# Performance work log

Measured on AMD Instinct MI355X. Metric: run time of the kernel, lower is better.

Reference implementation:

```python
import jax, jax.numpy as jnp
import numpy as np

N_NODES = 100000
N_FEAT = 256
HIDDEN = 16
N_CLASSES = 16
N_EDGES = 3200000


def setup_inputs() -> dict:
    key = jax.random.key(0)
    k = jax.random.split(key, 7)
    x = jax.random.normal(k[0], (N_NODES, N_FEAT), dtype=jnp.float32)
    edge_index = jax.random.randint(k[1], (2, N_EDGES), 0, N_NODES, dtype=jnp.int32)
    # GCNConv: linear (no bias) + bias added after aggregation
    s1 = 1.0 / np.sqrt(N_FEAT)
    W1 = jax.random.uniform(k[2], (N_FEAT, HIDDEN), jnp.float32, -s1, s1)
    b1 = jnp.zeros((HIDDEN,), jnp.float32)
    # SAGEConv: lin_l (on aggregated neighbors, with bias) + lin_r (root)
    s2 = 1.0 / np.sqrt(HIDDEN)
    Wl = jax.random.uniform(k[3], (HIDDEN, N_CLASSES), jnp.float32, -s2, s2)
    Wr = jax.random.uniform(k[4], (HIDDEN, N_CLASSES), jnp.float32, -s2, s2)
    b2 = jax.random.uniform(k[5], (N_CLASSES,), jnp.float32, -s2, s2)
    return {"x": x, "edge_index": edge_index, "W1": W1, "b1": b1,
            "Wl": Wl, "Wr": Wr, "b2": b2}


def reference(x, edge_index, W1, b1, Wl, Wr, b2):
    N = x.shape[0]
    src, dst = edge_index[0], edge_index[1]

    # ---- GCNConv(num_features -> hidden): transform, add self-loops,
    # symmetric normalization, sum-aggregate, add bias ----
    h = x @ W1  # [N, H]
    loop = jnp.arange(N, dtype=src.dtype)
    src2 = jnp.concatenate([src, loop])
    dst2 = jnp.concatenate([dst, loop])
    ones = jnp.ones(src2.shape[0], dtype=h.dtype)
    deg = jax.ops.segment_sum(ones, dst2, num_segments=N)  # in-degree incl. self-loop
    dinv = jnp.where(deg > 0, jax.lax.rsqrt(deg), 0.0)
    norm = dinv[src2] * dinv[dst2]  # [E+N]
    msgs = h[src2] * norm[:, None]
    h1 = jax.ops.segment_sum(msgs, dst2, num_segments=N) + b1  # [N, H]

    # ---- SAGEConv(hidden -> num_classes, aggr='mean') ----
    cnt = jax.ops.segment_sum(jnp.ones(src.shape[0], dtype=h1.dtype), dst, num_segments=N)
    agg = jax.ops.segment_sum(h1[src], dst, num_segments=N)
    agg = agg / jnp.maximum(cnt, 1.0)[:, None]  # mean over neighbors
    out = agg @ Wl + h1 @ Wr + b2  # [N, C]

    return jax.nn.log_softmax(out, axis=1)
```

## Files before the change

kernel.cpp:

```cpp
#include <hip/hip_runtime.h>
#include <cstddef>

#define NF 256
#define NH 16
#define NC 16

#define BN    128
#define BSH   7
#define BMSK  127
#define CAP   4608
#define AVLEN 32
#define ACH   (256*AVLEN)
#define NBMAX 800

typedef __attribute__((ext_vector_type(8))) short bf16x8;
typedef __attribute__((ext_vector_type(4))) float f32x4;

__device__ inline short f2bf(float f) {
    union { float f; unsigned int u; } v; v.f = f;
    const unsigned int r = v.u + 0x7FFFu + ((v.u >> 16) & 1u);
    return (short)(r >> 16);
}
__device__ inline float bf2f(unsigned short u) {
    union { unsigned int i; float f; } v; v.i = ((unsigned int)u) << 16;
    return v.f;
}

__global__ __launch_bounds__(256) void bucketA_kernel(
    const int* __restrict__ src, const int* __restrict__ dst,
    unsigned int* __restrict__ bfill, unsigned int* __restrict__ bpairs,
    int E, int NBK)
{
    __shared__ unsigned int hist[NBMAX];
    __shared__ unsigned int sbase[NBMAX];
    __shared__ unsigned int gpos[NBMAX];
    __shared__ unsigned int tmp[1024];
    __shared__ unsigned int reorder[ACH];
    __shared__ unsigned short wbid[ACH];

    const int tid = threadIdx.x;
    for (int i = tid; i < NBMAX; i += 256) hist[i] = 0u;
    __syncthreads();

    const int base = blockIdx.x * ACH;
    unsigned int pv[AVLEN];
    unsigned int ps[AVLEN];
    #pragma unroll
    for (int l = 0; l < AVLEN; ++l) {
        const int e = base + l * 256 + tid;
        if (e < E) {
            const unsigned int s = (unsigned int)src[e];
            const unsigned int d = (unsigned int)dst[e];
            const unsigned int b = d >> BSH;
            pv[l] = (s << BSH) | (d & BMSK);
            const unsigned int slot = atomicAdd(&hist[b], 1u);
            ps[l] = (slot << 10) | b;
        } else {
            ps[l] = 0xFFFFFFFFu;
        }
    }
    __syncthreads();

    for (int i = tid; i < 1024; i += 256) tmp[i] = (i < NBK) ? hist[i] : 0u;
    __syncthreads();
    for (int off = 1; off < 1024; off <<= 1) {
        unsigned int v0 = 0, v1 = 0, v2 = 0, v3 = 0;
        const int i0 = tid, i1 = tid + 256, i2 = tid + 512, i3 = tid + 768;
        if (i0 >= off) v0 = tmp[i0 - off];
        if (i1 >= off) v1 = tmp[i1 - off];
        if (i2 >= off) v2 = tmp[i2 - off];
        if (i3 >= off) v3 = tmp[i3 - off];
        __syncthreads();
        tmp[i0] += v0; tmp[i1] += v1; tmp[i2] += v2; tmp[i3] += v3;
        __syncthreads();
    }
    for (int i = tid; i < NBK; i += 256) {
        const unsigned int h = hist[i];
        sbase[i] = tmp[i] - h;
        if (h) gpos[i] = atomicAdd(&bfill[i], h);
    }
    const int cc = (base + ACH <= E) ? ACH : (E - base);
    __syncthreads();

    #pragma unroll
    for (int l = 0; l < AVLEN; ++l) {
        if (ps[l] != 0xFFFFFFFFu) {
            const unsigned int b = ps[l] & 1023u;
            const unsigned int i = sbase[b] + (ps[l] >> 10);
            reorder[i] = pv[l];
            wbid[i] = (unsigned short)b;
        }
    }
    __syncthreads();

    for (int i = tid; i < cc; i += 256) {
        const unsigned int b = wbid[i];
        const unsigned int g = gpos[b] + ((unsigned int)i - sbase[b]);
        if (g < CAP) bpairs[(size_t)b * CAP + g] = reorder[i];
    }
}

__global__ __launch_bounds__(256) void bucketB_kernel(
    const unsigned int* __restrict__ bfill, unsigned int* __restrict__ bpairs,
    int* __restrict__ rowptr, int* __restrict__ cnt, float* __restrict__ dinv,
    int N)
{
    __shared__ unsigned int pairs[CAP];
    __shared__ unsigned int ssorted[CAP];
    __shared__ unsigned int hist[BN];
    __shared__ unsigned int scan[BN];
    __shared__ unsigned int cursor[BN];

    const int tid = threadIdx.x;
    const int b = blockIdx.x;
    const size_t bbase = (size_t)b * CAP;
    unsigned int m = bfill[b]; if (m > CAP) m = CAP;

    if (tid < BN) hist[tid] = 0u;
    __syncthreads();

    for (unsigned int i = tid; i < m; i += 256) {
        const unsigned int p = bpairs[bbase + i];
        pairs[i] = p;
        atomicAdd(&hist[p & BMSK], 1u);
    }
    __syncthreads();

    if (tid < BN) scan[tid] = hist[tid];
    __syncthreads();
    for (int off = 1; off < BN; off <<= 1) {
        unsigned int v = 0;
        if (tid < BN && tid >= off) v = scan[tid - off];
        __syncthreads();
        if (tid < BN) scan[tid] += v;
        __syncthreads();
    }
    if (tid < BN) cursor[tid] = scan[tid] - hist[tid];
    __syncthreads();

    for (unsigned int i = tid; i < m; i += 256) {
        const unsigned int p = pairs[i];
        const unsigned int pos = atomicAdd(&cursor[p & BMSK], 1u);
        ssorted[pos] = p >> BSH;
    }
    __syncthreads();

    for (unsigned int i = tid; i < m; i += 256)
        bpairs[bbase + i] = ssorted[i];

    if (tid < BN) {
        const int n = b * BN + tid;
        if (n < N) {
            const unsigned int h = hist[tid];
            cnt[n] = (int)h;
            dinv[n] = rsqrtf((float)h + 1.0f);
            rowptr[n] = (int)(b * CAP + (scan[tid] - h));
        }
    }
}

__global__ __launch_bounds__(256) void gemm1_mfma_kernel(
    const float* __restrict__ x, const float* __restrict__ W1,
    const float* __restrict__ dinv, unsigned short* __restrict__ hs_bf, int N)
{
    const int lane = threadIdx.x & 63;
    const int wave = threadIdx.x >> 6;
    const int quad = lane >> 4;
    const int mn   = lane & 15;

    bf16x8 bfrag[8];
    #pragma unroll
    for (int kc = 0; kc < 8; ++kc) {
        #pragma unroll
        for (int j = 0; j < 8; ++j) {
            const int k = kc * 32 + quad * 8 + j;
            bfrag[kc][j] = f2bf(W1[k * NH + mn]);
        }
    }

    const int tile = blockIdx.x * 4 + wave;
    if (tile * 16 >= N) return;
    const int n0 = tile * 16;

    f32x4 acc = {0.f, 0.f, 0.f, 0.f};
    const float* xrow = x + (size_t)(n0 + mn) * NF + quad * 8;
    #pragma unroll
    for (int kc = 0; kc < 8; ++kc) {
        const float4 lo = *(const float4*)(xrow + kc * 32);
        const float4 hi = *(const float4*)(xrow + kc * 32 + 4);
        bf16x8 af;
        af[0] = f2bf(lo.x); af[1] = f2bf(lo.y); af[2] = f2bf(lo.z); af[3] = f2bf(lo.w);
        af[4] = f2bf(hi.x); af[5] = f2bf(hi.y); af[6] = f2bf(hi.z); af[7] = f2bf(hi.w);
        acc = __builtin_amdgcn_mfma_f32_16x16x32_bf16(af, bfrag[kc], acc, 0, 0, 0);
    }

    const float4 dv = *(const float4*)(dinv + n0 + quad * 4);
    const float d[4] = {dv.x, dv.y, dv.z, dv.w};
    #pragma unroll
    for (int r = 0; r < 4; ++r) {
        const int row = quad * 4 + r;
        hs_bf[(size_t)(n0 + row) * NH + mn] = (unsigned short)f2bf(acc[r] * d[r]);
    }
}

__global__ __launch_bounds__(256) void gcn_gather_kernel(
    const unsigned short* __restrict__ hs_bf, const unsigned int* __restrict__ csrc,
    const int* __restrict__ rowptr, const int* __restrict__ cnt,
    const float* __restrict__ dinv, const float* __restrict__ b1,
    unsigned short* __restrict__ h1_bf, int N)
{
    const int tid = threadIdx.x;
    const int n = blockIdx.x * 16 + (tid >> 4);
    if (n >= N) return;
    const int j = tid & 15;
    const int start = rowptr[n];
    const int end = start + cnt[n];

    float acc = bf2f(hs_bf[(size_t)n * NH + j]);
    int k = start;
    for (; k + 16 <= end; k += 16) {
        const int myi = (int)csrc[k + j];
        float s = 0.f;
        #pragma unroll
        for (int u = 0; u < 16; ++u) {
            const int sidx = __shfl(myi, u, 16);
            s += bf2f(hs_bf[(size_t)sidx * NH + j]);
        }
        acc += s;
    }
    for (; k < end; ++k)
        acc += bf2f(hs_bf[(size_t)csrc[k] * NH + j]);

    h1_bf[(size_t)n * NH + j] = (unsigned short)f2bf(b1[j] + dinv[n] * acc);
}

__global__ __launch_bounds__(256) void sage_out_kernel(
    const unsigned short* __restrict__ h1_bf, const unsigned int* __restrict__ csrc,
    const int* __restrict__ rowptr, const int* __restrict__ cnt,
    const float* __restrict__ Wl, const float* __restrict__ Wr,
    const float* __restrict__ b2, float* __restrict__ out, int N)
{
    __shared__ float wls[NH * NC];
    __shared__ float wrs[NH * NC];
    __shared__ float b2s[NC];
    const int tid = threadIdx.x;
    if (tid < NH * NC) { wls[tid] = Wl[tid]; wrs[tid] = Wr[tid]; }
    if (tid < NC) b2s[tid] = b2[tid];
    __syncthreads();

    const int n = blockIdx.x * 16 + (tid >> 4);
    if (n >= N) return;
    const int j = tid & 15;
    const int start = rowptr[n];
    const int deg = cnt[n];
    const int end = start + deg;

    float acc = 0.f;
    int k = start;
    for (; k + 16 <= end; k += 16) {
        const int myi = (int)csrc[k + j];
        float s = 0.f;
        #pragma unroll
        for (int u = 0; u < 16; ++u) {
            const int sidx = __shfl(myi, u, 16);
            s += bf2f(h1_bf[(size_t)sidx * NH + j]);
        }
        acc += s;
    }
    for (; k < end; ++k)
        acc += bf2f(h1_bf[(size_t)csrc[k] * NH + j]);

    const float aggj = acc / fmaxf((float)deg, 1.0f);
    const float h1j  = bf2f(h1_bf[(size_t)n * NH + j]);

    float o = b2s[j];
    #pragma unroll
    for (int kk = 0; kk < NH; ++kk) {
        const float a  = __shfl(aggj, kk, 16);
        const float hh = __shfl(h1j,  kk, 16);
        o += a * wls[kk * NC + j] + hh * wrs[kk * NC + j];
    }

    float m = o;
    #pragma unroll
    for (int off = 1; off < 16; off <<= 1) m = fmaxf(m, __shfl_xor(m, off, 16));
    const float ex = expf(o - m);
    float ssum = ex;
    #pragma unroll
    for (int off = 1; off < 16; off <<= 1) ssum += __shfl_xor(ssum, off, 16);

    out[(size_t)n * NC + j] = (o - m) - logf(ssum);
}

extern "C" void kernel_launch(void* const* d_in, const int* in_sizes, int n_in,
                              void* d_out, int out_size, void* d_ws, size_t ws_size,
                              hipStream_t stream)
{
    const float* x  = (const float*)d_in[0];
    const int*   ei = (const int*)d_in[1];
    const float* W1 = (const float*)d_in[2];
    const float* b1 = (const float*)d_in[3];
    const float* Wl = (const float*)d_in[4];
    const float* Wr = (const float*)d_in[5];
    const float* b2 = (const float*)d_in[6];
    float* out = (float*)d_out;

    const int N = in_sizes[0] / NF;
    const int E = in_sizes[1] / 2;
    const int* src = ei;
    const int* dst = ei + E;

    const int NBK = (N + BN - 1) / BN;

    unsigned short* hs_bf = (unsigned short*)d_ws;
    unsigned short* h1_bf = hs_bf + (size_t)N * NH;
    float* dinv   = (float*)(h1_bf + (size_t)N * NH);
    int*   cnt    = (int*)(dinv + N);
    int*   rowptr = cnt + N;
    unsigned int* bfill  = (unsigned int*)(rowptr + N);
    unsigned int* bpairs = bfill + 1024;

    hipMemsetAsync(bfill, 0, (size_t)NBK * sizeof(unsigned int), stream);

    bucketA_kernel<<<(E + ACH - 1) / ACH, 256, 0, stream>>>(src, dst, bfill, bpairs, E, NBK);
    bucketB_kernel<<<NBK, 256, 0, stream>>>(bfill, bpairs, rowptr, cnt, dinv, N);

    const int tiles = (N + 15) / 16;
    gemm1_mfma_kernel<<<(tiles + 3) / 4, 256, 0, stream>>>(x, W1, dinv, hs_bf, N);

    const int nodeBlk = (N + 15) / 16;
    gcn_gather_kernel<<<nodeBlk, 256, 0, stream>>>(hs_bf, bpairs, rowptr, cnt, dinv, b1, h1_bf, N);
    sage_out_kernel<<<nodeBlk, 256, 0, stream>>>(h1_bf, bpairs, rowptr, cnt, Wl, Wr, b2, out, N);
}
```

Measured before the change: 314.4 us.

## Replace per-node CSR sort with bucket-level LDS atomic aggregation

Drops the within-bucket counting sort and rowptr construction, keeping only a degree histogram pass. The two aggregation kernels now process one 128-node bucket per 512-thread block, scattering neighbor features into a shared-memory accumulator with LDS float atomics. This removes the sort's LDS work and global rewrite of bpairs, but adds LDS atomic contention and lowers the grid to about 800 blocks. It also makes float summation order nondeterministic.

```diff
diff --git a/kernel.cpp b/kernel.cpp
--- a/kernel.cpp
+++ b/kernel.cpp
@@ -100,53 +100,21 @@
     }
 }
 
-__global__ __launch_bounds__(256) void bucketB_kernel(
-    const unsigned int* __restrict__ bfill, unsigned int* __restrict__ bpairs,
-    int* __restrict__ rowptr, int* __restrict__ cnt, float* __restrict__ dinv,
-    int N)
-{
-    __shared__ unsigned int pairs[CAP];
-    __shared__ unsigned int ssorted[CAP];
+__global__ __launch_bounds__(256) void degree_kernel(
+    const unsigned int* __restrict__ bfill, const unsigned int* __restrict__ bpairs,
+    int* __restrict__ cnt, float* __restrict__ dinv, int N)
+{
     __shared__ unsigned int hist[BN];
-    __shared__ unsigned int scan[BN];
-    __shared__ unsigned int cursor[BN];
-
     const int tid = threadIdx.x;
     const int b = blockIdx.x;
+    if (tid < BN) hist[tid] = 0u;
+    __syncthreads();
+
+    unsigned int m = bfill[b]; if (m > CAP) m = CAP;
     const size_t bbase = (size_t)b * CAP;
-    unsigned int m = bfill[b]; if (m > CAP) m = CAP;
-
-    if (tid < BN) hist[tid] = 0u;
-    __syncthreads();
-
-    for (unsigned int i = tid; i < m; i += 256) {
-        const unsigned int p = bpairs[bbase + i];
-        pairs[i] = p;
-        atomicAdd(&hist[p & BMSK], 1u);
-    }
-    __syncthreads();
-
-    if (tid < BN) scan[tid] = hist[tid];
-    __syncthreads();
-    for (int off = 1; off < BN; off <<= 1) {
-        unsigned int v = 0;
-        if (tid < BN && tid >= off) v = scan[tid - off];
-        __syncthreads();
-        if (tid < BN) scan[tid] += v;
-        __syncthreads();
-    }
-    if (tid < BN) cursor[tid] = scan[tid] - hist[tid];
-    __syncthreads();
-
-    for (unsigned int i = tid; i < m; i += 256) {
-        const unsigned int p = pairs[i];
-        const unsigned int pos = atomicAdd(&cursor[p & BMSK], 1u);
-        ssorted[pos] = p >> BSH;
-    }
-    __syncthreads();
-
     for (unsigned int i = tid; i < m; i += 256)
-        bpairs[bbase + i] = ssorted[i];
+        atomicAdd(&hist[bpairs[bbase + i] & BMSK], 1u);
+    __syncthreads();
 
     if (tid < BN) {
         const int n = b * BN + tid;
@@ -154,7 +122,6 @@
             const unsigned int h = hist[tid];
             cnt[n] = (int)h;
             dinv[n] = rsqrtf((float)h + 1.0f);
-            rowptr[n] = (int)(b * CAP + (scan[tid] - h));
         }
     }
 }
@@ -203,93 +170,130 @@
     }
 }
 
-__global__ __launch_bounds__(256) void gcn_gather_kernel(
-    const unsigned short* __restrict__ hs_bf, const unsigned int* __restrict__ csrc,
-    const int* __restrict__ rowptr, const int* __restrict__ cnt,
+__global__ __launch_bounds__(512) void gcn_agg_kernel(
+    const unsigned short* __restrict__ hs_bf,
+    const unsigned int* __restrict__ bfill, const unsigned int* __restrict__ bpairs,
     const float* __restrict__ dinv, const float* __restrict__ b1,
     unsigned short* __restrict__ h1_bf, int N)
 {
+    __shared__ float acc[BN * NH];
     const int tid = threadIdx.x;
-    const int n = blockIdx.x * 16 + (tid >> 4);
-    if (n >= N) return;
+    const int b = blockIdx.x;
+    const size_t bbase = (size_t)b * CAP;
+    const int nodeBase = b * BN;
+
+    for (int t = tid; t < BN * NH; t += 512) {
+        const int n = nodeBase + (t >> 4);
+        acc[t] = (n < N) ? bf2f(hs_bf[(size_t)n * NH + (t & 15)]) : 0.f;
+    }
+    unsigned int m = bfill[b]; if (m > CAP) m = CAP;
+    __syncthreads();
+
+    const int g = tid >> 4;
     const int j = tid & 15;
-    const int start = rowptr[n];
-    const int end = start + cnt[n];
-
-    float acc = bf2f(hs_bf[(size_t)n * NH + j]);
-    int k = start;
-    for (; k + 16 <= end; k += 16) {
-        const int myi = (int)csrc[k + j];
-        float s = 0.f;
-        #pragma unroll
-        for (int u = 0; u < 16; ++u) {
-            const int sidx = __shfl(myi, u, 16);
-            s += bf2f(hs_bf[(size_t)sidx * NH + j]);
-        }
-        acc += s;
-    }
-    for (; k < end; ++k)
-        acc += bf2f(hs_bf[(size_t)csrc[k] * NH + j]);
-
-    h1_bf[(size_t)n * NH + j] = (unsigned short)f2bf(b1[j] + dinv[n] * acc);
-}
-
-__global__ __launch_bounds__(256) void sage_out_kernel(
-    const unsigned short* __restrict__ h1_bf, const unsigned int* __restrict__ csrc,
-    const int* __restrict__ rowptr, const int* __restrict__ cnt,
+    unsigned int i = g;
+    for (; i + 96 < m; i += 128) {
+        const unsigned int p0 = bpairs[bbase + i];
+        const unsigned int p1 = bpairs[bbase + i + 32];
+        const unsigned int p2 = bpairs[bbase + i + 64];
+        const unsigned int p3 = bpairs[bbase + i + 96];
+        const float v0 = bf2f(hs_bf[(size_t)(p0 >> BSH) * NH + j]);
+        const float v1 = bf2f(hs_bf[(size_t)(p1 >> BSH) * NH + j]);
+        const float v2 = bf2f(hs_bf[(size_t)(p2 >> BSH) * NH + j]);
+        const float v3 = bf2f(hs_bf[(size_t)(p3 >> BSH) * NH + j]);
+        atomicAdd(&acc[((p0 & BMSK) << 4) + j], v0);
+        atomicAdd(&acc[((p1 & BMSK) << 4) + j], v1);
+        atomicAdd(&acc[((p2 & BMSK) << 4) + j], v2);
+        atomicAdd(&acc[((p3 & BMSK) << 4) + j], v3);
+    }
+    for (; i < m; i += 32) {
+        const unsigned int p0 = bpairs[bbase + i];
+        const float v0 = bf2f(hs_bf[(size_t)(p0 >> BSH) * NH + j]);
+        atomicAdd(&acc[((p0 & BMSK) << 4) + j], v0);
+    }
+    __syncthreads();
+
+    for (int t = tid; t < BN * NH; t += 512) {
+        const int n = nodeBase + (t >> 4);
+        if (n < N)
+            h1_bf[(size_t)n * NH + (t & 15)] =
+                (unsigned short)f2bf(b1[t & 15] + dinv[n] * acc[t]);
+    }
+}
+
+__global__ __launch_bounds__(512) void sage_out_kernel(
+    const unsigned short* __restrict__ h1_bf,
+    const unsigned int* __restrict__ bfill, const unsigned int* __restrict__ bpairs,
+    const int* __restrict__ cnt,
     const float* __restrict__ Wl, const float* __restrict__ Wr,
     const float* __restrict__ b2, float* __restrict__ out, int N)
 {
+    __shared__ float acc[BN * NH];
+    __shared__ unsigned short hroot[BN * NH];
     __shared__ float wls[NH * NC];
     __shared__ float wrs[NH * NC];
     __shared__ float b2s[NC];
+
     const int tid = threadIdx.x;
+    const int b = blockIdx.x;
+    const size_t bbase = (size_t)b * CAP;
+    const int nodeBase = b * BN;
+
     if (tid < NH * NC) { wls[tid] = Wl[tid]; wrs[tid] = Wr[tid]; }
     if (tid < NC) b2s[tid] = b2[tid];
-    __syncthreads();
-
-    const int n = blockIdx.x * 16 + (tid >> 4);
-    if (n >= N) return;
+    for (int t = tid; t < BN * NH; t += 512) {
+        acc[t] = 0.f;
+        const int n = nodeBase + (t >> 4);
+        hroot[t] = (n < N) ? h1_bf[(size_t)n * NH + (t & 15)] : (unsigned short)0;
+    }
+    unsigned int m = bfill[b]; if (m > CAP) m = CAP;
+    __syncthreads();
+
+    const int g = tid >> 4;
     const int j = tid & 15;
-    const int start = rowptr[n];
-    const int deg = cnt[n];
-    const int end = start + deg;
-
-    float acc = 0.f;
-    int k = start;
-    for (; k + 16 <= end; k += 16) {
-        const int myi = (int)csrc[k + j];
-        float s = 0.f;
+    unsigned int i = g;
+    for (; i + 96 < m; i += 128) {
+        const unsigned int p0 = bpairs[bbase + i];
+        const unsigned int p1 = bpairs[bbase + i + 32];
+        const unsigned int p2 = bpairs[bbase + i + 64];
+        const unsigned int p3 = bpairs[bbase + i + 96];
+        const float v0 = bf2f(h1_bf[(size_t)(p0 >> BSH) * NH + j]);
+        const float v1 = bf2f(h1_bf[(size_t)(p1 >> BSH) * NH + j]);
+        const float v2 = bf2f(h1_bf[(size_t)(p2 >> BSH) * NH + j]);
+        const float v3 = bf2f(h1_bf[(size_t)(p3 >> BSH) * NH + j]);
+        atomicAdd(&acc[((p0 & BMSK) << 4) + j], v0);
+        atomicAdd(&acc[((p1 & BMSK) << 4) + j], v1);
+        atomicAdd(&acc[((p2 & BMSK) << 4) + j], v2);
+        atomicAdd(&acc[((p3 & BMSK) << 4) + j], v3);
+    }
+    for (; i < m; i += 32) {
+        const unsigned int p0 = bpairs[bbase + i];
+        const float v0 = bf2f(h1_bf[(size_t)(p0 >> BSH) * NH + j]);
+        atomicAdd(&acc[((p0 & BMSK) << 4) + j], v0);
+    }
+    __syncthreads();
+
+    for (int t = tid; t < BN * NH; t += 512) {
+        const int i2 = t >> 4;
+        const int n = nodeBase + i2;
+        if (n >= N) continue;
+        const int jj = t & 15;
+        const float inv = 1.0f / fmaxf((float)cnt[n], 1.0f);
+        float o = b2s[jj];
         #pragma unroll
-        for (int u = 0; u < 16; ++u) {
-            const int sidx = __shfl(myi, u, 16);
-            s += bf2f(h1_bf[(size_t)sidx * NH + j]);
-        }
-        acc += s;
-    }
-    for (; k < end; ++k)
-        acc += bf2f(h1_bf[(size_t)csrc[k] * NH + j]);
-
-    const float aggj = acc / fmaxf((float)deg, 1.0f);
-    const float h1j  = bf2f(h1_bf[(size_t)n * NH + j]);
-
-    float o = b2s[j];
-    #pragma unroll
-    for (int kk = 0; kk < NH; ++kk) {
-        const float a  = __shfl(aggj, kk, 16);
-        const float hh = __shfl(h1j,  kk, 16);
-        o += a * wls[kk * NC + j] + hh * wrs[kk * NC + j];
-    }
-
-    float m = o;
-    #pragma unroll
-    for (int off = 1; off < 16; off <<= 1) m = fmaxf(m, __shfl_xor(m, off, 16));
-    const float ex = expf(o - m);
-    float ssum = ex;
-    #pragma unroll
-    for (int off = 1; off < 16; off <<= 1) ssum += __shfl_xor(ssum, off, 16);
-
-    out[(size_t)n * NC + j] = (o - m) - logf(ssum);
+        for (int kk = 0; kk < NH; ++kk) {
+            o += acc[(i2 << 4) + kk] * inv * wls[kk * NC + jj]
+               + bf2f(hroot[(i2 << 4) + kk]) * wrs[kk * NC + jj];
+        }
+        float mx = o;
+        #pragma unroll
+        for (int off = 1; off < 16; off <<= 1) mx = fmaxf(mx, __shfl_xor(mx, off, 16));
+        const float ex = expf(o - mx);
+        float ssum = ex;
+        #pragma unroll
+        for (int off = 1; off < 16; off <<= 1) ssum += __shfl_xor(ssum, off, 16);
+        out[(size_t)n * NC + jj] = (o - mx) - logf(ssum);
+    }
 }
 
 extern "C" void kernel_launch(void* const* d_in, const int* in_sizes, int n_in,
@@ -316,19 +320,17 @@
     unsigned short* h1_bf = hs_bf + (size_t)N * NH;
     float* dinv   = (float*)(h1_bf + (size_t)N * NH);
     int*   cnt    = (int*)(dinv + N);
-    int*   rowptr = cnt + N;
-    unsigned int* bfill  = (unsigned int*)(rowptr + N);
+    unsigned int* bfill  = (unsigned int*)(cnt + N);
     unsigned int* bpairs = bfill + 1024;
 
     hipMemsetAsync(bfill, 0, (size_t)NBK * sizeof(unsigned int), stream);
 
     bucketA_kernel<<<(E + ACH - 1) / ACH, 256, 0, stream>>>(src, dst, bfill, bpairs, E, NBK);
-    bucketB_kernel<<<NBK, 256, 0, stream>>>(bfill, bpairs, rowptr, cnt, dinv, N);
+    degree_kernel<<<NBK, 256, 0, stream>>>(bfill, bpairs, cnt, dinv, N);
 
     const int tiles = (N + 15) / 16;
     gemm1_mfma_kernel<<<(tiles + 3) / 4, 256, 0, stream>>>(x, W1, dinv, hs_bf, N);
 
-    const int nodeBlk = (N + 15) / 16;
-    gcn_gather_kernel<<<nodeBlk, 256, 0, stream>>>(hs_bf, bpairs, rowptr, cnt, dinv, b1, h1_bf, N);
-    sage_out_kernel<<<nodeBlk, 256, 0, stream>>>(h1_bf, bpairs, rowptr, cnt, Wl, Wr, b2, out, N);
-}
+    gcn_agg_kernel<<<NBK, 512, 0, stream>>>(hs_bf, bfill, bpairs, dinv, b1, h1_bf, N);
+    sage_out_kernel<<<NBK, 512, 0, stream>>>(h1_bf, bfill, bpairs, cnt, Wl, Wr, b2, out, N);
+}
```

New measurement: 905.4 us. 188% more time.
